# Kernel optimization log

Hardware: AMD Instinct MI355X
Metric: run time of the kernel (lower is better)

Reference implementation:

```python
import jax, jax.numpy as jnp
import numpy as np

T, N, C, D, S = 512, 32, 1296, 512, 30
NORM_SCALE = 32.0
NEGINF = -1e9


def setup_inputs() -> dict:
    key = jax.random.key(0)
    k1, k2, k3, k4, k5 = jax.random.split(key, 5)
    feats = jax.random.normal(k1, (T * N, D), dtype=jnp.float32)
    classifier_weight = jax.random.normal(k2, (D, C), dtype=jnp.float32)
    labeling = jax.random.randint(k3, (N, S), 1, C)  # targets cannot be blank(0)
    logit_lgts = (T - jax.random.randint(k4, (N,), 0, 32)).astype(jnp.int32)
    labeling_lgts = (S - jax.random.randint(k5, (N,), 0, 5)).astype(jnp.int32)
    return dict(feats=feats, classifier_weight=classifier_weight,
                labeling=labeling, logit_lgts=logit_lgts, labeling_lgts=labeling_lgts)


def _ctc_loss(log_probs, labels, in_lens, lab_lens):
    # log_probs: (T, N, C); labels: (N, S); blank = 0; reduction = 'sum'
    Tt, Nn, Cc = log_probs.shape
    Ss = labels.shape[1]
    L = 2 * Ss + 1
    # extended labeling: blank, l1, blank, l2, ..., blank  -> (N, L)
    ext = jnp.zeros((Nn, L), dtype=labels.dtype).at[:, 1::2].set(labels)
    # gather per-state log-probs: (T, N, L)
    lp_ext = jnp.take_along_axis(log_probs, jnp.broadcast_to(ext[None], (Tt, Nn, L)), axis=2)
    # skip transition s-2 -> s allowed iff s > 1 and ext[s] != ext[s-2]
    skip_ok = jnp.concatenate(
        [jnp.zeros((Nn, 2), dtype=bool), ext[:, 2:] != ext[:, :-2]], axis=1)
    alpha0 = (jnp.full((Nn, L), NEGINF, dtype=log_probs.dtype)
              .at[:, 0].set(lp_ext[0, :, 0])
              .at[:, 1].set(lp_ext[0, :, 1]))

    def step(alpha, inp):
        lp_t, t = inp  # lp_t: (N, L)
        a1 = alpha
        a2 = jnp.pad(alpha[:, :-1], ((0, 0), (1, 0)), constant_values=NEGINF)
        a3 = jnp.where(skip_ok,
                       jnp.pad(alpha[:, :-2], ((0, 0), (2, 0)), constant_values=NEGINF),
                       NEGINF)
        new = jax.nn.logsumexp(jnp.stack([a1, a2, a3], axis=0), axis=0) + lp_t
        # freeze alpha once t reaches a sample's input length
        alpha = jnp.where((t < in_lens)[:, None], new, alpha)
        return alpha, None

    alpha, _ = jax.lax.scan(step, alpha0, (lp_ext[1:], jnp.arange(1, Tt)))
    Ln = 2 * lab_lens + 1  # (N,)
    last = jnp.take_along_axis(alpha, (Ln - 1)[:, None], axis=1)[:, 0]
    last2 = jnp.take_along_axis(alpha, (Ln - 2)[:, None], axis=1)[:, 0]
    nll = -jnp.logaddexp(last, last2)
    return jnp.sum(nll)


def reference(feats, classifier_weight, labeling, logit_lgts, labeling_lgts):
    # RadialCTC: cosine logits with norm_scale, then CTC on log-softmax.
    w_n = classifier_weight / jnp.linalg.norm(classifier_weight, axis=0, keepdims=True)  # (D, C)
    f_n = feats / jnp.linalg.norm(feats, axis=1, keepdims=True)  # (T*N, D)
    logits = NORM_SCALE * (f_n @ w_n)  # (T*N, C)
    log_probs = jax.nn.log_softmax(logits.reshape(T, N, C), axis=-1)
    return _ctc_loss(log_probs, labeling, logit_lgts, labeling_lgts)
```

## Files before the change

### kernel.cpp

```cpp
#include <hip/hip_runtime.h>
#include <stdint.h>
#include <stddef.h>


typedef _Float16 f16;
typedef _Float16 f16x8 __attribute__((ext_vector_type(8)));
typedef float f32x4 __attribute__((ext_vector_type(4)));
typedef __attribute__((address_space(1))) void* as1_void_ptr;
typedef __attribute__((address_space(3))) void* as3_void_ptr;

#define TT 512
#define NN 32
#define CC 1296
#define DD 512
#define SS 30
#define CP 1408
#define LL 61
#define NEGINF (-1e9f)
#define NORM_SCALE 32.0f
#define LOG2E 1.4426950408889634f
#define LN2   0.6931471805599453f

#define PREP_WBLK (CP / 16)
#define PREP_ZBLK 17
#define PREP_FBLK (TT * NN / 4)

__device__ __forceinline__ float fexp2(float x) { return __builtin_amdgcn_exp2f(x); }
__device__ __forceinline__ float flog2(float x) { return __builtin_amdgcn_logf(x); }

__device__ __forceinline__ double dpp_sr1_zero64(double x) {
    long long b = __double_as_longlong(x);
    int lo = (int)(b & 0xFFFFFFFFLL);
    int hi = (int)(b >> 32);
    int lo2 = __builtin_amdgcn_update_dpp(0, lo, 0x138, 0xF, 0xF, false);
    int hi2 = __builtin_amdgcn_update_dpp(0, hi, 0x138, 0xF, 0xF, false);
    return __longlong_as_double(((long long)hi2 << 32) |
                                (unsigned long long)(unsigned int)lo2);
}
template <int CTRL>
__device__ __forceinline__ int dpp_imax_level(int m) {
    int t = __builtin_amdgcn_update_dpp(0, m, CTRL, 0xF, 0xF, false);
    return m > t ? m : t;
}

__global__ __launch_bounds__(256) void prep_kernel(const float* __restrict__ W,
                                                   const float* __restrict__ feats,
                                                   f16* __restrict__ wt,
                                                   f16* __restrict__ fn,
                                                   float* __restrict__ sumexp,
                                                   unsigned* __restrict__ ctr) {
    int bx = blockIdx.x, tid = threadIdx.x;
    if (bx < PREP_WBLK) {
        __shared__ float red[256];
        __shared__ float rqs[16];
        int c0 = bx * 16;
        int cl = tid & 15, dg = tid >> 4;
        int c = c0 + cl;
        float ss = 0.f;
        if (c < CC) {
            for (int d = dg; d < DD; d += 16) {
                float v = W[(size_t)d * CC + c];
                ss += v * v;
            }
        }
        red[tid] = ss;
        __syncthreads();
        if (tid < 16) {
            float s2 = 0.f;
            #pragma unroll
            for (int k = 0; k < 16; ++k) s2 += red[tid + 16 * k];
            rqs[tid] = rsqrtf(s2);
        }
        __syncthreads();
        int c_loc = tid >> 4, dl = tid & 15;
        int cc = c0 + c_loc;
        float rq = rqs[c_loc];
        #pragma unroll 4
        for (int it = 0; it < 32; ++it) {
            int d = dl + it * 16;
            float v = (cc < CC) ? W[(size_t)d * CC + cc] * rq : 0.f;
            wt[(size_t)cc * DD + d] = (f16)v;
        }
    } else if (bx < PREP_WBLK + PREP_ZBLK) {
        int zb = bx - PREP_WBLK;
        if (zb < 16) {
            float4 z = {0.f, 0.f, 0.f, 0.f};
            ((float4*)sumexp)[zb * 256 + tid] = z;
        } else if (tid == 0) {
            *ctr = 0u;
        }
    } else {
        int fb = bx - PREP_WBLK - PREP_ZBLK;
        int wv = (fb * 256 + tid) >> 6;
        int lane = tid & 63;
        const float4* src = (const float4*)(feats + (size_t)wv * DD) + lane * 2;
        float4 a = src[0], b = src[1];
        float ss = a.x*a.x + a.y*a.y + a.z*a.z + a.w*a.w
                 + b.x*b.x + b.y*b.y + b.z*b.z + b.w*b.w;
        #pragma unroll
        for (int off = 32; off; off >>= 1) ss += __shfl_xor(ss, off);
        float r = rsqrtf(ss);
        f16x8 o;
        o[0]=(f16)(a.x*r); o[1]=(f16)(a.y*r); o[2]=(f16)(a.z*r); o[3]=(f16)(a.w*r);
        o[4]=(f16)(b.x*r); o[5]=(f16)(b.y*r); o[6]=(f16)(b.z*r); o[7]=(f16)(b.w*r);
        *(f16x8*)(fn + (size_t)wv * DD + lane * 8) = o;
    }
}

__global__ __launch_bounds__(256) void gemm_sumexp_kernel(const f16* __restrict__ A,
                                                          const f16* __restrict__ B,
                                                          float* __restrict__ sumexp) {
    __shared__ __align__(16) f16 As[128 * 32];
    __shared__ __align__(16) f16 Bs[128 * 32];
    int bm = blockIdx.x, bn = blockIdx.y;
    int tid = threadIdx.x;
    int w = tid >> 6, lane = tid & 63;
    int wm = w >> 1, wn = w & 1;
    int lm = lane & 15, hi = lane >> 4;
    int sw = (lm >> 1) & 3;
    f32x4 acc[4][4];
    f32x4 zero = {0.f, 0.f, 0.f, 0.f};
    #pragma unroll
    for (int i = 0; i < 4; ++i)
        #pragma unroll
        for (int j = 0; j < 4; ++j) acc[i][j] = zero;

    for (int kb = 0; kb < 16; ++kb) {
        #pragma unroll
        for (int p = 0; p < 2; ++p) {
            int s = p * 256 + tid;
            int row = s >> 2;
            int ch = (s & 3) ^ ((row >> 1) & 3);
            const f16* ga = A + (size_t)(bm * 128 + row) * DD + kb * 32 + ch * 8;
            const f16* gb = B + (size_t)(bn * 128 + row) * DD + kb * 32 + ch * 8;
            __builtin_amdgcn_global_load_lds((as1_void_ptr)ga,
                (as3_void_ptr)&As[(p * 256 + w * 64) * 8], 16, 0, 0);
            __builtin_amdgcn_global_load_lds((as1_void_ptr)gb,
                (as3_void_ptr)&Bs[(p * 256 + w * 64) * 8], 16, 0, 0);
        }
        __syncthreads();
        f16x8 af[4], bf[4];
        #pragma unroll
        for (int i = 0; i < 4; ++i)
            af[i] = *(const f16x8*)&As[(wm * 64 + i * 16 + lm) * 32 + (hi ^ sw) * 8];
        #pragma unroll
        for (int j = 0; j < 4; ++j)
            bf[j] = *(const f16x8*)&Bs[(wn * 64 + j * 16 + lm) * 32 + (hi ^ sw) * 8];
        #pragma unroll
        for (int i = 0; i < 4; ++i)
            #pragma unroll
            for (int j = 0; j < 4; ++j)
                acc[i][j] = __builtin_amdgcn_mfma_f32_16x16x32_f16(af[i], bf[j], acc[i][j], 0, 0, 0);
        __syncthreads();
    }
    #pragma unroll
    for (int i = 0; i < 4; ++i) {
        float rs[4] = {0.f, 0.f, 0.f, 0.f};
        #pragma unroll
        for (int j = 0; j < 4; ++j) {
            int c = bn * 128 + wn * 64 + j * 16 + lm;
            bool ok = (c < CC);
            #pragma unroll
            for (int r = 0; r < 4; ++r)
                rs[r] += ok ? fexp2(acc[i][j][r] * (NORM_SCALE * LOG2E)) : 0.f;
        }
        #pragma unroll
        for (int off = 1; off < 16; off <<= 1) {
            #pragma unroll
            for (int r = 0; r < 4; ++r) rs[r] += __shfl_xor(rs[r], off);
        }
        if (lm == 0) {
            int rowb = bm * 128 + wm * 64 + i * 16 + hi * 4;
            #pragma unroll
            for (int r = 0; r < 4; ++r) atomicAdd(&sumexp[rowb + r], rs[r]);
        }
    }
}

__global__ __launch_bounds__(256) void gather_kernel(const f16* __restrict__ fn,
                                                     const f16* __restrict__ wt,
                                                     const float* __restrict__ sumexp,
                                                     const int* __restrict__ labels,
                                                     float* __restrict__ lp_lab) {
    __shared__ __align__(16) f16 Bs[16 * 32 * 32];
    __shared__ __align__(16) f16 As[16 * 64 * 32];
    __shared__ float ls2[64];
    int n = blockIdx.x, t0 = blockIdx.y * 64;
    int tid = threadIdx.x;
    int w = tid >> 6, lane = tid & 63;
    int lm = lane & 15, hi = lane >> 4;
    int sw = (lm >> 1) & 3;

    #pragma unroll
    for (int it = 0; it < 8; ++it) {
        int s = it * 256 + tid;
        int row = (s >> 2) & 31;
        int ch = (s & 3) ^ ((row >> 1) & 3);
        int cls = (row == 0 || row > SS) ? 0 : labels[n * SS + row - 1];
        const f16* gb = wt + (size_t)cls * DD + (s >> 7) * 32 + ch * 8;
        __builtin_amdgcn_global_load_lds((as1_void_ptr)gb,
            (as3_void_ptr)&Bs[(it * 256 + w * 64) * 8], 16, 0, 0);
    }
    #pragma unroll
    for (int it = 0; it < 16; ++it) {
        int s = it * 256 + tid;
        int kb = s >> 8, row = (s >> 2) & 63;
        int ch = (s & 3) ^ ((row >> 1) & 3);
        const f16* ga = fn + (size_t)((t0 + row) * NN + n) * DD + kb * 32 + ch * 8;
        __builtin_amdgcn_global_load_lds((as1_void_ptr)ga,
            (as3_void_ptr)&As[(it * 256 + w * 64) * 8], 16, 0, 0);
    }
    if (tid < 64) ls2[tid] = flog2(sumexp[(size_t)(t0 + tid) * NN + n]);
    __syncthreads();

    f32x4 acc[2];
    acc[0] = (f32x4){0.f, 0.f, 0.f, 0.f};
    acc[1] = (f32x4){0.f, 0.f, 0.f, 0.f};
    #pragma unroll
    for (int kb = 0; kb < 16; ++kb) {
        f16x8 af  = *(const f16x8*)&As[kb * 2048 + (w * 16 + lm) * 32 + (hi ^ sw) * 8];
        f16x8 bf0 = *(const f16x8*)&Bs[kb * 1024 + lm * 32 + (hi ^ sw) * 8];
        f16x8 bf1 = *(const f16x8*)&Bs[kb * 1024 + (16 + lm) * 32 + (hi ^ sw) * 8];
        acc[0] = __builtin_amdgcn_mfma_f32_16x16x32_f16(af, bf0, acc[0], 0, 0, 0);
        acc[1] = __builtin_amdgcn_mfma_f32_16x16x32_f16(af, bf1, acc[1], 0, 0, 0);
    }
    #pragma unroll
    for (int jn = 0; jn < 2; ++jn) {
        int j = jn * 16 + lm;
        if (j >= 31) continue;
        float* dst = lp_lab + ((size_t)n * 31 + j) * TT + t0;
        #pragma unroll
        for (int r = 0; r < 4; ++r) {
            int tl = w * 16 + hi * 4 + r;
            dst[tl] = acc[jn][r] * (NORM_SCALE * LOG2E) - ls2[tl];
        }
    }
}

__global__ void ctc_kernel(const float* __restrict__ lp_lab, const int* __restrict__ labels,
                           const int* __restrict__ in_lens, const int* __restrict__ lab_lens,
                           float* __restrict__ nll, unsigned* __restrict__ ctr,
                           float* __restrict__ out) {
    int n = blockIdx.x;
    int s = threadIdx.x;
    bool valid = s < LL;
    int ext = (valid && (s & 1)) ? labels[n * SS + (s >> 1)] : 0;
    int jmap = (valid && (s & 1)) ? ((s >> 1) + 1) : 0;
    int ext2 = __shfl_up(ext, 2);
    double skipd = ((s >= 2) && valid && (ext != ext2)) ? 1.0 : 0.0;
    int Tin = in_lens[n];
    const float4* g0 = (const float4*)(lp_lab + ((size_t)n * 31 + jmap) * TT);

    float4 cur = g0[0];
    float4 nxt = g0[1];
    float4 nx2 = g0[2];
    double beta = (s <= 1) ? (double)fexp2(cur.x) : 0.0;
    int Mi = 0;

    auto stepL = [&](float lp) {
        double P = (double)fexp2(lp);
        double b1 = dpp_sr1_zero64(beta);
        double b2 = dpp_sr1_zero64(b1);
        beta = (beta + b1 + b2 * skipd) * P;
    };
    auto renorm = [&]() {
        int h = (int)(__double_as_longlong(beta) >> 32);
        h = dpp_imax_level<0x111>(h);
        h = dpp_imax_level<0x112>(h);
        h = dpp_imax_level<0x114>(h);
        h = dpp_imax_level<0x118>(h);
        int r0 = __builtin_amdgcn_readlane(h, 15);
        int r1 = __builtin_amdgcn_readlane(h, 31);
        int r2 = __builtin_amdgcn_readlane(h, 47);
        int r3 = __builtin_amdgcn_readlane(h, 63);
        int mx = max(max(r0, r1), max(r2, r3));
        int e11 = mx >> 20;
        double scale = __longlong_as_double((long long)(2046 - e11) << 52);
        beta *= scale;
        Mi += e11 - 1023;
    };

    stepL(cur.y); stepL(cur.z); stepL(cur.w);
    renorm();
    int remaining = Tin - 4;
    int g = 1;
    while (remaining >= 4) {
        cur = nxt; nxt = nx2;
        int gi = g + 2; if (gi > 127) gi = 127;
        nx2 = g0[gi];
        stepL(cur.x); stepL(cur.y); stepL(cur.z); stepL(cur.w);
        renorm();
        remaining -= 4; ++g;
    }
    cur = nxt;
    if (remaining > 0) stepL(cur.x);
    if (remaining > 1) stepL(cur.y);
    if (remaining > 2) stepL(cur.z);

    int Ln = 2 * lab_lens[n] + 1;
    double last  = __shfl(beta, Ln - 1);
    double last2 = __shfl(beta, Ln - 2);
    double sm = last + last2;
    long long bb = __double_as_longlong(sm);
    int e = (int)(bb >> 52) - 1023;
    double mant = __longlong_as_double((bb & 0xFFFFFFFFFFFFFLL) | (1023LL << 52));
    float v = -(flog2((float)mant) + (float)(e + Mi)) * LN2;
    if (s == 0) {
        nll[n] = v;
        __threadfence();
        unsigned old = atomicAdd(ctr, 1u);
        if (old == NN - 1) {
            __threadfence();
            float t = 0.f;
            for (int i = 0; i < NN; ++i) t += nll[i];
            out[0] = t;
        }
    }
}

extern "C" void kernel_launch(void* const* d_in, const int* in_sizes, int n_in,
                              void* d_out, int out_size, void* d_ws, size_t ws_size,
                              hipStream_t stream) {
    const float* feats        = (const float*)d_in[0];
    const float* W            = (const float*)d_in[1];
    const int*   labeling     = (const int*)d_in[2];
    const int*   logit_lgts   = (const int*)d_in[3];
    const int*   labeling_lgts= (const int*)d_in[4];
    float* out = (float*)d_out;
    char* ws = (char*)d_ws;

    size_t off = 0;
    f16*   wt     = (f16*)(ws + off);   off += (size_t)CP * DD * 2;
    f16*   fn     = (f16*)(ws + off);   off += (size_t)TT * NN * DD * 2;
    float* sumexp = (float*)(ws + off); off += (size_t)TT * NN * 4;
    float* lp_lab = (float*)(ws + off); off += (size_t)NN * 31 * TT * 4;
    float* nllb   = (float*)(ws + off); off += 64 * 4;
    unsigned* ctr = (unsigned*)(ws + off); off += 64;

    prep_kernel<<<PREP_WBLK + PREP_ZBLK + PREP_FBLK, 256, 0, stream>>>(
        W, feats, wt, fn, sumexp, ctr);
    gemm_sumexp_kernel<<<dim3(TT * NN / 128, CP / 128), 256, 0, stream>>>(fn, wt, sumexp);
    gather_kernel<<<dim3(NN, TT / 64), 256, 0, stream>>>(fn, wt, sumexp, labeling, lp_lab);
    ctc_kernel<<<NN, 64, 0, stream>>>(lp_lab, labeling, logit_lgts, labeling_lgts,
                                      nllb, ctr, out);

    (void)in_sizes; (void)n_in; (void)out_size; (void)ws_size;
}
```

Baseline: 162.9 us.

## Merge GEMM and label-gather kernels by deferring log-normalizer subtraction to CTC

The per-frame log-sum-exp term is constant across all CTC states at a given time step, so it factors out of the alpha recursion and can be summed over valid frames at the end. That removes the gather kernel's dependency on the completed sumexp, so the gather blocks are launched in the same grid as the GEMM/sumexp blocks, saving one launch and the serialization between them. The gather path now streams K in 32-wide chunks through a small shared buffer instead of preloading everything. The CTC kernel picks up an extra reduction over the valid frames' log-normalizers, done in double, to keep precision.

Measured after the change: 160.7 us. No clear change (-1.4%).

```diff
diff --git a/kernel.cpp b/kernel.cpp
--- a/kernel.cpp
+++ b/kernel.cpp
@@ -16,7 +16,6 @@
 #define SS 30
 #define CP 1408
 #define LL 61
-#define NEGINF (-1e9f)
 #define NORM_SCALE 32.0f
 #define LOG2E 1.4426950408889634f
 #define LN2   0.6931471805599453f
@@ -24,6 +23,9 @@
 #define PREP_WBLK (CP / 16)
 #define PREP_ZBLK 17
 #define PREP_FBLK (TT * NN / 4)
+
+#define GEMM_BLK ((TT * NN / 128) * (CP / 128))
+#define GATH_BLK (NN * (TT / 64))
 
 __device__ __forceinline__ float fexp2(float x) { return __builtin_amdgcn_exp2f(x); }
 __device__ __forceinline__ float flog2(float x) { return __builtin_amdgcn_logf(x); }
@@ -107,138 +109,123 @@
     }
 }
 
-__global__ __launch_bounds__(256) void gemm_sumexp_kernel(const f16* __restrict__ A,
-                                                          const f16* __restrict__ B,
-                                                          float* __restrict__ sumexp) {
-    __shared__ __align__(16) f16 As[128 * 32];
-    __shared__ __align__(16) f16 Bs[128 * 32];
-    int bm = blockIdx.x, bn = blockIdx.y;
-    int tid = threadIdx.x;
-    int w = tid >> 6, lane = tid & 63;
-    int wm = w >> 1, wn = w & 1;
-    int lm = lane & 15, hi = lane >> 4;
-    int sw = (lm >> 1) & 3;
-    f32x4 acc[4][4];
-    f32x4 zero = {0.f, 0.f, 0.f, 0.f};
-    #pragma unroll
-    for (int i = 0; i < 4; ++i)
-        #pragma unroll
-        for (int j = 0; j < 4; ++j) acc[i][j] = zero;
-
-    for (int kb = 0; kb < 16; ++kb) {
-        #pragma unroll
-        for (int p = 0; p < 2; ++p) {
-            int s = p * 256 + tid;
-            int row = s >> 2;
-            int ch = (s & 3) ^ ((row >> 1) & 3);
-            const f16* ga = A + (size_t)(bm * 128 + row) * DD + kb * 32 + ch * 8;
-            const f16* gb = B + (size_t)(bn * 128 + row) * DD + kb * 32 + ch * 8;
-            __builtin_amdgcn_global_load_lds((as1_void_ptr)ga,
-                (as3_void_ptr)&As[(p * 256 + w * 64) * 8], 16, 0, 0);
-            __builtin_amdgcn_global_load_lds((as1_void_ptr)gb,
-                (as3_void_ptr)&Bs[(p * 256 + w * 64) * 8], 16, 0, 0);
-        }
-        __syncthreads();
-        f16x8 af[4], bf[4];
-        #pragma unroll
-        for (int i = 0; i < 4; ++i)
-            af[i] = *(const f16x8*)&As[(wm * 64 + i * 16 + lm) * 32 + (hi ^ sw) * 8];
-        #pragma unroll
-        for (int j = 0; j < 4; ++j)
-            bf[j] = *(const f16x8*)&Bs[(wn * 64 + j * 16 + lm) * 32 + (hi ^ sw) * 8];
-        #pragma unroll
-        for (int i = 0; i < 4; ++i)
-            #pragma unroll
-            for (int j = 0; j < 4; ++j)
-                acc[i][j] = __builtin_amdgcn_mfma_f32_16x16x32_f16(af[i], bf[j], acc[i][j], 0, 0, 0);
-        __syncthreads();
-    }
-    #pragma unroll
-    for (int i = 0; i < 4; ++i) {
-        float rs[4] = {0.f, 0.f, 0.f, 0.f};
-        #pragma unroll
-        for (int j = 0; j < 4; ++j) {
-            int c = bn * 128 + wn * 64 + j * 16 + lm;
-            bool ok = (c < CC);
-            #pragma unroll
-            for (int r = 0; r < 4; ++r)
-                rs[r] += ok ? fexp2(acc[i][j][r] * (NORM_SCALE * LOG2E)) : 0.f;
-        }
-        #pragma unroll
-        for (int off = 1; off < 16; off <<= 1) {
-            #pragma unroll
-            for (int r = 0; r < 4; ++r) rs[r] += __shfl_xor(rs[r], off);
-        }
-        if (lm == 0) {
-            int rowb = bm * 128 + wm * 64 + i * 16 + hi * 4;
-            #pragma unroll
-            for (int r = 0; r < 4; ++r) atomicAdd(&sumexp[rowb + r], rs[r]);
-        }
-    }
-}
-
-__global__ __launch_bounds__(256) void gather_kernel(const f16* __restrict__ fn,
-                                                     const f16* __restrict__ wt,
-                                                     const float* __restrict__ sumexp,
-                                                     const int* __restrict__ labels,
-                                                     float* __restrict__ lp_lab) {
-    __shared__ __align__(16) f16 Bs[16 * 32 * 32];
-    __shared__ __align__(16) f16 As[16 * 64 * 32];
-    __shared__ float ls2[64];
-    int n = blockIdx.x, t0 = blockIdx.y * 64;
+__global__ __launch_bounds__(256) void gg_kernel(const f16* __restrict__ A,
+                                                 const f16* __restrict__ B,
+                                                 const int* __restrict__ labels,
+                                                 float* __restrict__ sumexp,
+                                                 float* __restrict__ lp_lab) {
+    __shared__ __align__(16) f16 sm[8192];
+    int bx = blockIdx.x;
     int tid = threadIdx.x;
     int w = tid >> 6, lane = tid & 63;
     int lm = lane & 15, hi = lane >> 4;
     int sw = (lm >> 1) & 3;
 
-    #pragma unroll
-    for (int it = 0; it < 8; ++it) {
-        int s = it * 256 + tid;
-        int row = (s >> 2) & 31;
-        int ch = (s & 3) ^ ((row >> 1) & 3);
-        int cls = (row == 0 || row > SS) ? 0 : labels[n * SS + row - 1];
-        const f16* gb = wt + (size_t)cls * DD + (s >> 7) * 32 + ch * 8;
-        __builtin_amdgcn_global_load_lds((as1_void_ptr)gb,
-            (as3_void_ptr)&Bs[(it * 256 + w * 64) * 8], 16, 0, 0);
-    }
-    #pragma unroll
-    for (int it = 0; it < 16; ++it) {
-        int s = it * 256 + tid;
-        int kb = s >> 8, row = (s >> 2) & 63;
-        int ch = (s & 3) ^ ((row >> 1) & 3);
-        const f16* ga = fn + (size_t)((t0 + row) * NN + n) * DD + kb * 32 + ch * 8;
-        __builtin_amdgcn_global_load_lds((as1_void_ptr)ga,
-            (as3_void_ptr)&As[(it * 256 + w * 64) * 8], 16, 0, 0);
-    }
-    if (tid < 64) ls2[tid] = flog2(sumexp[(size_t)(t0 + tid) * NN + n]);
-    __syncthreads();
-
-    f32x4 acc[2];
-    acc[0] = (f32x4){0.f, 0.f, 0.f, 0.f};
-    acc[1] = (f32x4){0.f, 0.f, 0.f, 0.f};
-    #pragma unroll
-    for (int kb = 0; kb < 16; ++kb) {
-        f16x8 af  = *(const f16x8*)&As[kb * 2048 + (w * 16 + lm) * 32 + (hi ^ sw) * 8];
-        f16x8 bf0 = *(const f16x8*)&Bs[kb * 1024 + lm * 32 + (hi ^ sw) * 8];
-        f16x8 bf1 = *(const f16x8*)&Bs[kb * 1024 + (16 + lm) * 32 + (hi ^ sw) * 8];
-        acc[0] = __builtin_amdgcn_mfma_f32_16x16x32_f16(af, bf0, acc[0], 0, 0, 0);
-        acc[1] = __builtin_amdgcn_mfma_f32_16x16x32_f16(af, bf1, acc[1], 0, 0, 0);
-    }
-    #pragma unroll
-    for (int jn = 0; jn < 2; ++jn) {
-        int j = jn * 16 + lm;
-        if (j >= 31) continue;
-        float* dst = lp_lab + ((size_t)n * 31 + j) * TT + t0;
+    if (bx < GEMM_BLK) {
+        int bm = bx & 127, bn = bx >> 7;
+        int wm = w >> 1, wn = w & 1;
+        f32x4 acc[4][4];
+        f32x4 zero = {0.f, 0.f, 0.f, 0.f};
         #pragma unroll
-        for (int r = 0; r < 4; ++r) {
-            int tl = w * 16 + hi * 4 + r;
-            dst[tl] = acc[jn][r] * (NORM_SCALE * LOG2E) - ls2[tl];
+        for (int i = 0; i < 4; ++i)
+            #pragma unroll
+            for (int j = 0; j < 4; ++j) acc[i][j] = zero;
+
+        for (int kb = 0; kb < 16; ++kb) {
+            #pragma unroll
+            for (int p = 0; p < 2; ++p) {
+                int s = p * 256 + tid;
+                int row = s >> 2;
+                int ch = (s & 3) ^ ((row >> 1) & 3);
+                const f16* ga = A + (size_t)(bm * 128 + row) * DD + kb * 32 + ch * 8;
+                const f16* gb = B + (size_t)(bn * 128 + row) * DD + kb * 32 + ch * 8;
+                __builtin_amdgcn_global_load_lds((as1_void_ptr)ga,
+                    (as3_void_ptr)&sm[(p * 256 + w * 64) * 8], 16, 0, 0);
+                __builtin_amdgcn_global_load_lds((as1_void_ptr)gb,
+                    (as3_void_ptr)&sm[4096 + (p * 256 + w * 64) * 8], 16, 0, 0);
+            }
+            __syncthreads();
+            f16x8 af[4], bf[4];
+            #pragma unroll
+            for (int i = 0; i < 4; ++i)
+                af[i] = *(const f16x8*)&sm[(wm * 64 + i * 16 + lm) * 32 + (hi ^ sw) * 8];
+            #pragma unroll
+            for (int j = 0; j < 4; ++j)
+                bf[j] = *(const f16x8*)&sm[4096 + (wn * 64 + j * 16 + lm) * 32 + (hi ^ sw) * 8];
+            #pragma unroll
+            for (int i = 0; i < 4; ++i)
+                #pragma unroll
+                for (int j = 0; j < 4; ++j)
+                    acc[i][j] = __builtin_amdgcn_mfma_f32_16x16x32_f16(af[i], bf[j], acc[i][j], 0, 0, 0);
+            __syncthreads();
+        }
+        #pragma unroll
+        for (int i = 0; i < 4; ++i) {
+            float rs[4] = {0.f, 0.f, 0.f, 0.f};
+            #pragma unroll
+            for (int j = 0; j < 4; ++j) {
+                int c = bn * 128 + wn * 64 + j * 16 + lm;
+                bool ok = (c < CC);
+                #pragma unroll
+                for (int r = 0; r < 4; ++r)
+                    rs[r] += ok ? fexp2(acc[i][j][r] * (NORM_SCALE * LOG2E)) : 0.f;
+            }
+            #pragma unroll
+            for (int off = 1; off < 16; off <<= 1) {
+                #pragma unroll
+                for (int r = 0; r < 4; ++r) rs[r] += __shfl_xor(rs[r], off);
+            }
+            if (lm == 0) {
+                int rowb = bm * 128 + wm * 64 + i * 16 + hi * 4;
+                #pragma unroll
+                for (int r = 0; r < 4; ++r) atomicAdd(&sumexp[rowb + r], rs[r]);
+            }
+        }
+    } else {
+        int gbx = bx - GEMM_BLK;
+        int n = gbx & 31, t0 = (gbx >> 5) * 64;
+        int arow = tid >> 2;
+        int ach = (tid & 3) ^ ((arow >> 1) & 3);
+        const f16* gaB = A + (size_t)((t0 + arow) * NN + n) * DD + ach * 8;
+        int brow = tid >> 2;
+        int bch = (tid & 3) ^ ((brow >> 1) & 3);
+        int cls = (brow == 0 || brow > SS) ? 0 : labels[n * SS + brow - 1];
+        const f16* gbB = B + (size_t)cls * DD + bch * 8;
+
+        f32x4 acc0 = {0.f, 0.f, 0.f, 0.f};
+        f32x4 acc1 = {0.f, 0.f, 0.f, 0.f};
+        for (int kb = 0; kb < 16; ++kb) {
+            __builtin_amdgcn_global_load_lds((as1_void_ptr)(gaB + kb * 32),
+                (as3_void_ptr)&sm[tid * 8], 16, 0, 0);
+            if (tid < 128)
+                __builtin_amdgcn_global_load_lds((as1_void_ptr)(gbB + kb * 32),
+                    (as3_void_ptr)&sm[2048 + tid * 8], 16, 0, 0);
+            __syncthreads();
+            f16x8 af  = *(const f16x8*)&sm[(w * 16 + lm) * 32 + (hi ^ sw) * 8];
+            f16x8 bf0 = *(const f16x8*)&sm[2048 + lm * 32 + (hi ^ sw) * 8];
+            f16x8 bf1 = *(const f16x8*)&sm[2048 + (16 + lm) * 32 + (hi ^ sw) * 8];
+            acc0 = __builtin_amdgcn_mfma_f32_16x16x32_f16(af, bf0, acc0, 0, 0, 0);
+            acc1 = __builtin_amdgcn_mfma_f32_16x16x32_f16(af, bf1, acc1, 0, 0, 0);
+            __syncthreads();
+        }
+        #pragma unroll
+        for (int jn = 0; jn < 2; ++jn) {
+            int j = jn * 16 + lm;
+            if (j >= 31) continue;
+            float* dst = lp_lab + ((size_t)n * 31 + j) * TT + t0;
+            f32x4 av = jn ? acc1 : acc0;
+            #pragma unroll
+            for (int r = 0; r < 4; ++r) {
+                int tl = w * 16 + hi * 4 + r;
+                dst[tl] = av[r] * (NORM_SCALE * LOG2E);
+            }
         }
     }
 }
 
 __global__ void ctc_kernel(const float* __restrict__ lp_lab, const int* __restrict__ labels,
                            const int* __restrict__ in_lens, const int* __restrict__ lab_lens,
+                           const float* __restrict__ sumexp,
                            float* __restrict__ nll, unsigned* __restrict__ ctr,
                            float* __restrict__ out) {
     int n = blockIdx.x;
@@ -297,6 +284,12 @@
     if (remaining > 1) stepL(cur.y);
     if (remaining > 2) stepL(cur.z);
 
+    double ms = 0.0;
+    for (int t = s; t < Tin; t += 64)
+        ms += (double)flog2(sumexp[(size_t)t * NN + n]);
+    #pragma unroll
+    for (int off = 32; off; off >>= 1) ms += __shfl_xor(ms, off);
+
     int Ln = 2 * lab_lens[n] + 1;
     double last  = __shfl(beta, Ln - 1);
     double last2 = __shfl(beta, Ln - 2);
@@ -304,7 +297,7 @@
     long long bb = __double_as_longlong(sm);
     int e = (int)(bb >> 52) - 1023;
     double mant = __longlong_as_double((bb & 0xFFFFFFFFFFFFFLL) | (1023LL << 52));
-    float v = -(flog2((float)mant) + (float)(e + Mi)) * LN2;
+    float v = (float)(-((double)flog2((float)mant) + (double)(e + Mi) - ms) * LN2);
     if (s == 0) {
         nll[n] = v;
         __threadfence();
@@ -339,10 +332,9 @@
 
     prep_kernel<<<PREP_WBLK + PREP_ZBLK + PREP_FBLK, 256, 0, stream>>>(
         W, feats, wt, fn, sumexp, ctr);
-    gemm_sumexp_kernel<<<dim3(TT * NN / 128, CP / 128), 256, 0, stream>>>(fn, wt, sumexp);
-    gather_kernel<<<dim3(NN, TT / 64), 256, 0, stream>>>(fn, wt, sumexp, labeling, lp_lab);
+    gg_kernel<<<GEMM_BLK + GATH_BLK, 256, 0, stream>>>(fn, wt, labeling, sumexp, lp_lab);
     ctc_kernel<<<NN, 64, 0, stream>>>(lp_lab, labeling, logit_lgts, labeling_lgts,
-                                      nllb, ctr, out);
+                                      sumexp, nllb, ctr, out);
 
     (void)in_sizes; (void)n_in; (void)out_size; (void)ws_size;
 }
```
